# Kernel tuning notes

Hardware: AMD Instinct MI355X
Metric: run time of the kernel (lower is better)

The kernel has to match this reference:

```python
import jax, jax.numpy as jnp
import numpy as np

B, S = 2, 4096
H, D = 8, 64      # num_heads, per-head embed_dim
W = 128           # window (even)
O = 64            # num_outputs per head
ZERO_VALUE = 0.0


def setup_inputs() -> dict:
    key = jax.random.key(0)
    kq, kk, kv, kwq, kwk, kbq, kbk, ko = jax.random.split(key, 8)
    scale = 1.0 / np.sqrt(D)
    return {
        "q": jax.random.normal(kq, (B, S, H * D), dtype=jnp.float32),
        "k": jax.random.normal(kk, (B, S, H * D), dtype=jnp.float32),
        "v": jax.random.normal(kv, (B, S, H * O), dtype=jnp.float32),
        "Wq": jax.random.normal(kwq, (D, D), dtype=jnp.float32) * scale,
        "bq": jax.random.normal(kbq, (D,), dtype=jnp.float32) * 0.02,
        "Wk": jax.random.normal(kwk, (D, D), dtype=jnp.float32) * scale,
        "bk": jax.random.normal(kbk, (D,), dtype=jnp.float32) * 0.02,
        "ocpe": jax.random.normal(ko, (W + 1, H), dtype=jnp.float32) * 0.02,
    }


def reference(q, k, v, Wq, bq, Wk, bk, ocpe):
    b, s, _ = q.shape
    p = W // 2
    assert s % W == 0
    C = s // W  # number of chunks of size `window`

    # split heads + per-head projections (nn.Linear: x @ W.T + b)
    q = q.reshape(b, s, H, D) @ Wq.T + bq
    k = k.reshape(b, s, H, D) @ Wk.T + bk
    v = v.reshape(b, s, H, O)

    # pad seq dim by window//2 on both sides (matches F.pad in source)
    qp = jnp.pad(q, ((0, 0), (p, p), (0, 0), (0, 0)))
    kp = jnp.pad(k, ((0, 0), (p, p), (0, 0), (0, 0)))
    vp = jnp.pad(v, ((0, 0), (p, p), (0, 0), (0, 0)))

    # overlapping chunks of length 2W (chunk_size=W plus 2*p halo)
    starts = jnp.arange(C) * W                 # (C,)
    loc = jnp.arange(2 * W)                    # (2W,)
    idx = starts[:, None] + loc[None, :]       # (C, 2W) indices into padded seq
    qc = qp[:, idx]                            # (B, C, 2W, H, D)
    kc = kp[:, idx]
    vc = vp[:, idx]                            # (B, C, 2W, H, O)

    scores = jnp.einsum('ncxhd,ncyhd->ncxyh', qc, kc)  # (B,C,2W,2W,H)

    diff = loc[None, :] - loc[:, None]         # j - i, (2W, 2W)
    within = jnp.abs(diff) <= p                # (2W, 2W)
    bias = jnp.where(within[:, :, None],
                     ocpe[jnp.clip(p + diff, 0, W)], 0.0)  # (2W,2W,H)
    scores = scores + bias[None, None]

    # boundary mask: global padded position must lie in [p, s+p)
    pos = starts[:, None] + loc[None, :]       # (C, 2W)
    valid = (pos >= p) & (pos < s + p)         # (C, 2W)
    mask = within[None] & valid[:, :, None] & valid[:, None, :]  # (C,2W,2W)

    scores = jnp.where(mask[None, :, :, :, None], scores, ZERO_VALUE)
    attn = jnp.tanh(scores)

    res = jnp.einsum('ncxyh,ncyhd->ncxd', attn, vc)  # (B,C,2W,O)
    out = res[:, :, p:2 * W - p].reshape(b, s, O)     # middle W rows per chunk

    # attn_flat[b,c,i,d,h] = attn[b,c, i+p, i+d, h]
    r = jnp.arange(W)
    rows = r[:, None] + p                      # (W, 1)
    cols = r[:, None] + jnp.arange(W + 1)[None]  # (W, W+1)
    attn_flat = attn[:, :, rows, cols, :]      # (B, C, W, W+1, H)
    attn_flat = attn_flat.reshape(b, s, W + 1, H)
    return attn_flat, out
```

## Files before the change

### kernel.cpp

```cpp
#include <hip/hip_runtime.h>
#include <cstddef>

#define SB 2
#define SS 4096
#define SH 8
#define SD 64
#define SP 64
#define SNO 129
#define TQ 16
#define WN 144
#define NT16 (SS/TQ)
#define SSTR 168

typedef _Float16 f16;
typedef __attribute__((ext_vector_type(8))) _Float16 f16x8;
typedef __attribute__((ext_vector_type(4))) float floatx4;

union f16frag { f16 h[8]; ushort4 u4[2]; f16x8 v; };

__device__ __forceinline__ float fast_tanh(float x) {
  float ax = fabsf(x);
  float e = __expf(2.0f * ax);
  float t = 1.0f - 2.0f / (e + 1.0f);
  return copysignf(t, x);
}

__device__ __forceinline__ void cvt16(const float* __restrict__ src, f16* __restrict__ dst) {
  float4 x0 = *(const float4*)(src);
  float4 x1 = *(const float4*)(src + 4);
  float4 x2 = *(const float4*)(src + 8);
  float4 x3 = *(const float4*)(src + 12);
  f16frag a, c;
  a.h[0]=(f16)x0.x; a.h[1]=(f16)x0.y; a.h[2]=(f16)x0.z; a.h[3]=(f16)x0.w;
  a.h[4]=(f16)x1.x; a.h[5]=(f16)x1.y; a.h[6]=(f16)x1.z; a.h[7]=(f16)x1.w;
  c.h[0]=(f16)x2.x; c.h[1]=(f16)x2.y; c.h[2]=(f16)x2.z; c.h[3]=(f16)x2.w;
  c.h[4]=(f16)x3.x; c.h[5]=(f16)x3.y; c.h[6]=(f16)x3.z; c.h[7]=(f16)x3.w;
  *(ushort4*)(dst)      = a.u4[0];
  *(ushort4*)(dst + 4)  = a.u4[1];
  *(ushort4*)(dst + 8)  = c.u4[0];
  *(ushort4*)(dst + 12) = c.u4[1];
}

__global__ __launch_bounds__(256) void prep_kernel(
    const float* __restrict__ q, const float* __restrict__ k, const float* __restrict__ v,
    const float* __restrict__ Wq, const float* __restrict__ bq,
    const float* __restrict__ Wk, const float* __restrict__ bk,
    f16* __restrict__ Qf, f16* __restrict__ Kf, f16* __restrict__ Vt)
{
  __shared__ f16 sWq[64*72], sWk[64*72], sQr[64*72], sKr[64*72], sVr[64*72];
  __shared__ float sbq[64], sbk[64];

  int t = threadIdx.x;
  int blk = blockIdx.x;
  int c = blk & 63; int bh = blk >> 6; int h = bh & 7; int b = bh >> 3;
  int s0 = c * 64;

  int dr = t >> 2, e0 = (t & 3) * 16;
  cvt16(Wq + dr*64 + e0, &sWq[dr*72 + e0]);
  cvt16(Wk + dr*64 + e0, &sWk[dr*72 + e0]);
  {
    size_t rbase = ((size_t)(b*SS + s0 + dr)) * (SH*SD) + h*SD + e0;
    cvt16(q + rbase, &sQr[dr*72 + e0]);
    cvt16(k + rbase, &sKr[dr*72 + e0]);
    cvt16(v + rbase, &sVr[dr*72 + e0]);
  }
  if (t < 64) { sbq[t] = bq[t]; sbk[t] = bk[t]; }
  __syncthreads();

  int lane = t & 63, wave = t >> 6;
  int r16 = lane & 15, g = lane >> 4;

  size_t hsbase = (size_t)(b*SH + h) * SS;

  #pragma unroll
  for (int j = 0; j < 4; ++j) {
    int tt = wave + 4*j;
    int si = tt >> 2, dj = tt & 3;
    floatx4 accq = {0.f,0.f,0.f,0.f}, acck = {0.f,0.f,0.f,0.f};
    #pragma unroll
    for (int e = 0; e < 64; e += 32) {
      f16x8 aq = *(const f16x8*)&sQr[(si*16 + r16)*72 + e + g*8];
      f16x8 ak = *(const f16x8*)&sKr[(si*16 + r16)*72 + e + g*8];
      f16x8 wq8 = *(const f16x8*)&sWq[(dj*16 + r16)*72 + e + g*8];
      f16x8 wk8 = *(const f16x8*)&sWk[(dj*16 + r16)*72 + e + g*8];
      accq = __builtin_amdgcn_mfma_f32_16x16x32_f16(aq, wq8, accq, 0, 0, 0);
      acck = __builtin_amdgcn_mfma_f32_16x16x32_f16(ak, wk8, acck, 0, 0, 0);
    }
    float biasq = sbq[dj*16 + r16];
    float biask = sbk[dj*16 + r16];
    #pragma unroll
    for (int rr = 0; rr < 4; ++rr) {
      int srow = s0 + si*16 + g*4 + rr;
      Qf[(hsbase + srow)*64 + dj*16 + r16] = (f16)(accq[rr] + biasq);
      Kf[(hsbase + srow)*64 + dj*16 + r16] = (f16)(acck[rr] + biask);
    }
  }

  {
    int d = t >> 2, p4 = t & 3, sc0 = p4 * 16;
    f16frag a, c2;
    #pragma unroll
    for (int j2 = 0; j2 < 8; ++j2) a.h[j2] = sVr[(sc0 + j2)*72 + d];
    #pragma unroll
    for (int j2 = 0; j2 < 8; ++j2) c2.h[j2] = sVr[(sc0 + 8 + j2)*72 + d];
    f16* dst = Vt + ((size_t)(b*SH + h)*64 + d)*SS + s0 + sc0;
    *(ushort4*)dst       = a.u4[0];
    *(ushort4*)(dst + 4) = a.u4[1];
    *(ushort4*)(dst + 8) = c2.u4[0];
    *(ushort4*)(dst + 12)= c2.u4[1];
  }
}

__global__ __launch_bounds__(512, 4) void attn_fused(
    const f16* __restrict__ Qf, const f16* __restrict__ Kf, const f16* __restrict__ Vt,
    const float* __restrict__ ocpe, float* __restrict__ af, float* __restrict__ outp)
{
  __shared__ f16 sPriv[SH][TQ*SSTR];
  __shared__ f16 sAF[TQ*SNO*SH];
  __shared__ float sObT[SH*SNO];

  int t = threadIdx.x;
  int lane = t & 63, wave = t >> 6;
  int r16 = lane & 15, g = lane >> 4;

  int blk = blockIdx.x;
  int G = (blk & 7) * 64 + (blk >> 3);
  int b = G >> 8, t16 = G & 255;
  int t0 = t16 * TQ, yg0 = t0 - SP;

  for (int idx = t; idx < SNO*SH; idx += 512) {
    int o = idx >> 3, h2 = idx & 7;
    sObT[h2*SNO + o] = ocpe[idx];
  }

  int h = wave;
  f16* priv = &sPriv[wave][0];
  #pragma unroll
  for (int j = 0; j < 4; ++j)
    priv[r16*SSTR + WN + g*4 + j] = (f16)0.f;

  __syncthreads();

  const float* ob = &sObT[h*SNO];
  const f16* qb = Qf + ((size_t)(b*SH + h)*SS + t0 + r16)*64;
  f16x8 qa0 = *(const f16x8*)(qb + g*8);
  f16x8 qa1 = *(const f16x8*)(qb + 32 + g*8);
  const f16* kbase = Kf + ((size_t)(b*SH + h)*SS)*64;

  #pragma unroll
  for (int yy = 0; yy < 9; ++yy) {
    int y = yy*16 + r16;
    int ygr = yg0 + y;
    int ygc = min(max(ygr, 0), SS-1);
    bool yok = (ygr >= 0) & (ygr < SS);
    const f16* kr = kbase + (size_t)ygc * 64;
    f16x8 kb0 = *(const f16x8*)(kr + g*8);
    f16x8 kb1 = *(const f16x8*)(kr + 32 + g*8);
    floatx4 acc = {0.f,0.f,0.f,0.f};
    acc = __builtin_amdgcn_mfma_f32_16x16x32_f16(qa0, kb0, acc, 0, 0, 0);
    acc = __builtin_amdgcn_mfma_f32_16x16x32_f16(qa1, kb1, acc, 0, 0, 0);
    #pragma unroll
    for (int rr = 0; rr < 4; ++rr) {
      int i = g*4 + rr;
      int o = y - i;
      bool ook = (o >= 0) & (o <= 2*SP);
      float a = 0.f;
      if (yok & ook) a = fast_tanh(acc[rr] + ob[o]);
      priv[i*SSTR + y] = (f16)a;
      if (ook) sAF[((size_t)i*SNO + o)*SH + h] = (f16)a;
    }
  }

  floatx4 acc2[4] = {{0.f,0.f,0.f,0.f},{0.f,0.f,0.f,0.f},{0.f,0.f,0.f,0.f},{0.f,0.f,0.f,0.f}};
  const f16* vb0 = Vt + ((size_t)(b*SH + h)*64 + r16)*SS;
  #pragma unroll
  for (int ks = 0; ks < 5; ++ks) {
    int yb = ks*32 + g*8;
    int ygr = yg0 + yb;
    int ygc = min(max(ygr, 0), SS-8);
    f16x8 a0 = *(const f16x8*)&priv[r16*SSTR + yb];
    #pragma unroll
    for (int dq = 0; dq < 4; ++dq) {
      f16x8 bv = *(const f16x8*)(vb0 + (size_t)(dq*16)*SS + ygc);
      acc2[dq] = __builtin_amdgcn_mfma_f32_16x16x32_f16(a0, bv, acc2[dq], 0, 0, 0);
    }
  }

  {
    float* po = (float*)priv;
    #pragma unroll
    for (int dq = 0; dq < 4; ++dq)
      #pragma unroll
      for (int rr = 0; rr < 4; ++rr)
        po[(g*4 + rr)*64 + dq*16 + r16] = acc2[dq][rr];
  }

  __syncthreads();

  {
    int e2 = t * 2;
    int i = e2 >> 6, d = e2 & 63;
    float sx = 0.f, sy = 0.f;
    #pragma unroll
    for (int h2 = 0; h2 < SH; ++h2) {
      const float* ph = (const float*)&sPriv[h2][0];
      sx += ph[i*64 + d];
      sy += ph[i*64 + d + 1];
    }
    *(float2*)(outp + ((size_t)b*SS + t0 + i)*64 + d) = make_float2(sx, sy);
  }

  {
    float* afb = af + ((size_t)b*SS + t0) * (size_t)(SNO*SH);
    for (int idx = t; idx < TQ*SNO*SH/4; idx += 512) {
      const f16* s = &sAF[idx*4];
      float4 w = make_float4((float)s[0], (float)s[1], (float)s[2], (float)s[3]);
      *(float4*)(afb + idx*4) = w;
    }
  }
}

extern "C" void kernel_launch(void* const* d_in, const int* in_sizes, int n_in,
                              void* d_out, int out_size, void* d_ws, size_t ws_size,
                              hipStream_t stream) {
  const float* q    = (const float*)d_in[0];
  const float* k    = (const float*)d_in[1];
  const float* v    = (const float*)d_in[2];
  const float* Wq   = (const float*)d_in[3];
  const float* bq   = (const float*)d_in[4];
  const float* Wk   = (const float*)d_in[5];
  const float* bk   = (const float*)d_in[6];
  const float* ocpe = (const float*)d_in[7];

  f16* Kf = (f16*)d_ws;
  f16* Vt = Kf + (size_t)SB*SH*SS*SD;
  f16* Qf = Vt + (size_t)SB*SH*SS*SD;

  float* af = (float*)d_out;
  float* op = af + (size_t)SB*SS*SNO*SH;

  prep_kernel<<<SB*SH*64, 256, 0, stream>>>(q, k, v, Wq, bq, Wk, bk, Qf, Kf, Vt);
  attn_fused<<<SB*NT16, 512, 0, stream>>>(Qf, Kf, Vt, ocpe, af, op);
}
```

Before: 44.78 us.

## Use two waves per head, drop sAF buffer, reduce output via LDS atomics

Doubles the attention block to 1024 threads, with two waves per head splitting the score tiles and then the output columns. The separate sAF half-precision staging buffer is removed, and the attn_flat output is gathered directly from the per-head probability tiles. The cross-head sum of the output now uses shared-memory atomicAdd into a padded buffer instead of a serial reduction over eight heads. This cuts LDS footprint and per-wave work to raise parallelism, in exchange for an extra barrier, LDS atomics and a strided gather with integer division in the store loop.

```diff
diff --git a/kernel.cpp b/kernel.cpp
--- a/kernel.cpp
+++ b/kernel.cpp
@@ -11,6 +11,7 @@
 #define WN 144
 #define NT16 (SS/TQ)
 #define SSTR 168
+#define PRIV (TQ*SSTR + 8)
 
 typedef _Float16 f16;
 typedef __attribute__((ext_vector_type(8))) _Float16 f16x8;
@@ -111,33 +112,36 @@
   }
 }
 
-__global__ __launch_bounds__(512, 4) void attn_fused(
+__global__ __launch_bounds__(1024, 8) void attn_fused(
     const f16* __restrict__ Qf, const f16* __restrict__ Kf, const f16* __restrict__ Vt,
     const float* __restrict__ ocpe, float* __restrict__ af, float* __restrict__ outp)
 {
-  __shared__ f16 sPriv[SH][TQ*SSTR];
-  __shared__ f16 sAF[TQ*SNO*SH];
+  __shared__ f16 sPriv[SH*PRIV];
+  __shared__ float sOut[TQ*68];
   __shared__ float sObT[SH*SNO];
 
   int t = threadIdx.x;
   int lane = t & 63, wave = t >> 6;
   int r16 = lane & 15, g = lane >> 4;
+  int h = wave >> 1, half = wave & 1;
 
   int blk = blockIdx.x;
   int G = (blk & 7) * 64 + (blk >> 3);
   int b = G >> 8, t16 = G & 255;
   int t0 = t16 * TQ, yg0 = t0 - SP;
 
-  for (int idx = t; idx < SNO*SH; idx += 512) {
+  for (int idx = t; idx < SNO*SH; idx += 1024) {
     int o = idx >> 3, h2 = idx & 7;
     sObT[h2*SNO + o] = ocpe[idx];
   }
-
-  int h = wave;
-  f16* priv = &sPriv[wave][0];
-  #pragma unroll
-  for (int j = 0; j < 4; ++j)
-    priv[r16*SSTR + WN + g*4 + j] = (f16)0.f;
+  for (int idx = t; idx < TQ*68; idx += 1024) sOut[idx] = 0.f;
+
+  f16* priv = &sPriv[h*PRIV];
+  if (half == 0) {
+    #pragma unroll
+    for (int j = 0; j < 4; ++j)
+      priv[r16*SSTR + WN + g*4 + j] = (f16)0.f;
+  }
 
   __syncthreads();
 
@@ -147,8 +151,8 @@
   f16x8 qa1 = *(const f16x8*)(qb + 32 + g*8);
   const f16* kbase = Kf + ((size_t)(b*SH + h)*SS)*64;
 
-  #pragma unroll
-  for (int yy = 0; yy < 9; ++yy) {
+  int yBeg = half ? 5 : 0, yEnd = half ? 9 : 5;
+  for (int yy = yBeg; yy < yEnd; ++yy) {
     int y = yy*16 + r16;
     int ygr = yg0 + y;
     int ygc = min(max(ygr, 0), SS-1);
@@ -167,12 +171,13 @@
       float a = 0.f;
       if (yok & ook) a = fast_tanh(acc[rr] + ob[o]);
       priv[i*SSTR + y] = (f16)a;
-      if (ook) sAF[((size_t)i*SNO + o)*SH + h] = (f16)a;
-    }
-  }
-
-  floatx4 acc2[4] = {{0.f,0.f,0.f,0.f},{0.f,0.f,0.f,0.f},{0.f,0.f,0.f,0.f},{0.f,0.f,0.f,0.f}};
-  const f16* vb0 = Vt + ((size_t)(b*SH + h)*64 + r16)*SS;
+    }
+  }
+
+  __syncthreads();
+
+  floatx4 acc2[2] = {{0.f,0.f,0.f,0.f},{0.f,0.f,0.f,0.f}};
+  const f16* vb0 = Vt + ((size_t)(b*SH + h)*64 + half*32 + r16)*SS;
   #pragma unroll
   for (int ks = 0; ks < 5; ++ks) {
     int yb = ks*32 + g*8;
@@ -180,42 +185,40 @@
     int ygc = min(max(ygr, 0), SS-8);
     f16x8 a0 = *(const f16x8*)&priv[r16*SSTR + yb];
     #pragma unroll
-    for (int dq = 0; dq < 4; ++dq) {
+    for (int dq = 0; dq < 2; ++dq) {
       f16x8 bv = *(const f16x8*)(vb0 + (size_t)(dq*16)*SS + ygc);
       acc2[dq] = __builtin_amdgcn_mfma_f32_16x16x32_f16(a0, bv, acc2[dq], 0, 0, 0);
     }
   }
 
-  {
-    float* po = (float*)priv;
-    #pragma unroll
-    for (int dq = 0; dq < 4; ++dq)
-      #pragma unroll
-      for (int rr = 0; rr < 4; ++rr)
-        po[(g*4 + rr)*64 + dq*16 + r16] = acc2[dq][rr];
-  }
-
-  __syncthreads();
-
-  {
-    int e2 = t * 2;
-    int i = e2 >> 6, d = e2 & 63;
-    float sx = 0.f, sy = 0.f;
-    #pragma unroll
-    for (int h2 = 0; h2 < SH; ++h2) {
-      const float* ph = (const float*)&sPriv[h2][0];
-      sx += ph[i*64 + d];
-      sy += ph[i*64 + d + 1];
-    }
-    *(float2*)(outp + ((size_t)b*SS + t0 + i)*64 + d) = make_float2(sx, sy);
+  #pragma unroll
+  for (int dq = 0; dq < 2; ++dq)
+    #pragma unroll
+    for (int rr = 0; rr < 4; ++rr)
+      atomicAdd(&sOut[(g*4 + rr)*68 + half*32 + dq*16 + r16], acc2[dq][rr]);
+
+  __syncthreads();
+
+  if (t < TQ*SD) {
+    int i = t >> 6, d = t & 63;
+    outp[((size_t)b*SS + t0 + i)*64 + d] = sOut[i*68 + d];
   }
 
   {
     float* afb = af + ((size_t)b*SS + t0) * (size_t)(SNO*SH);
-    for (int idx = t; idx < TQ*SNO*SH/4; idx += 512) {
-      const f16* s = &sAF[idx*4];
-      float4 w = make_float4((float)s[0], (float)s[1], (float)s[2], (float)s[3]);
-      *(float4*)(afb + idx*4) = w;
+    const int NF4 = TQ*SNO*SH/4;
+    for (int fidx = t; fidx < NF4; fidx += 1024) {
+      int hq = (fidx & 1) * 4;
+      int oi = fidx >> 1;
+      int i = oi / SNO;
+      int o = oi - i * SNO;
+      const f16* s = &sPriv[hq*PRIV + i*SSTR + i + o];
+      float4 w;
+      w.x = (float)s[0*PRIV];
+      w.y = (float)s[1*PRIV];
+      w.z = (float)s[2*PRIV];
+      w.w = (float)s[3*PRIV];
+      *(float4*)(afb + (size_t)fidx*4) = w;
     }
   }
 }
@@ -240,5 +243,5 @@
   float* op = af + (size_t)SB*SS*SNO*SH;
 
   prep_kernel<<<SB*SH*64, 256, 0, stream>>>(q, k, v, Wq, bq, Wk, bk, Qf, Kf, Vt);
-  attn_fused<<<SB*NT16, 512, 0, stream>>>(Qf, Kf, Vt, ocpe, af, op);
-}
+  attn_fused<<<SB*NT16, 1024, 0, stream>>>(Qf, Kf, Vt, ocpe, af, op);
+}
```

After: 62.03 us. 1.39x slower.
